# Performance work log

Hardware: AMD Instinct MI355X
Metric: run time of the kernel (lower is better)

The kernel has to match this reference:

```python
import jax, jax.numpy as jnp
import numpy as np

N = 50000
E = 800000
IN_C = 128
HID = 128
OUT_C = 2


def _linear_params(key, fan_in, fan_out):
    k1, k2 = jax.random.split(key)
    bound = 1.0 / np.sqrt(fan_in)
    W = jax.random.uniform(k1, (fan_in, fan_out), jnp.float32, -bound, bound)
    b = jax.random.uniform(k2, (fan_out,), jnp.float32, -bound, bound)
    return W, b


def setup_inputs() -> dict:
    key = jax.random.key(0)
    ks = jax.random.split(key, 9)
    x = jax.random.normal(ks[0], (N, IN_C), jnp.float32)
    edge_index = jax.random.randint(ks[1], (2, E), 0, N, jnp.int64)
    W1a, b1a = _linear_params(ks[2], IN_C, HID)
    W1b, b1b = _linear_params(ks[3], HID, HID)
    W2a, b2a = _linear_params(ks[4], HID, HID)
    W2b, b2b = _linear_params(ks[5], HID, HID)
    Wfc, bfc = _linear_params(ks[6], HID, OUT_C)
    return {
        "x": x, "edge_index": edge_index,
        "W1a": W1a, "b1a": b1a, "W1b": W1b, "b1b": b1b,
        "W2a": W2a, "b2a": b2a, "W2b": W2b, "b2b": b2b,
        "Wfc": Wfc, "bfc": bfc,
    }


def _gin_conv(x, src, dst, Wa, ba, Wb, bb):
    # GINConv with eps=0: h = MLP(x + sum_{j in N(i)} x_j)
    agg = jax.ops.segment_sum(x[src], dst, num_segments=N)  # [N, d]
    h = x + agg
    h = jax.nn.relu(h @ Wa + ba)
    return h @ Wb + bb


def reference(x, edge_index, W1a, b1a, W1b, b1b, W2a, b2a, W2b, b2b, Wfc, bfc):
    src, dst = edge_index[0], edge_index[1]  # messages flow src -> dst
    h = _gin_conv(x, src, dst, W1a, b1a, W1b, b1b)
    h = jax.nn.relu(h)
    # dropout is identity in eval mode
    h = _gin_conv(h, src, dst, W2a, b2a, W2b, b2b)
    return h @ Wfc + bfc  # [N, 2]
```

## Files before the change

### kernel.cpp

```cpp
#include <hip/hip_runtime.h>

#define N_NODES 50000
#define N_EDGES 800000
#define NBUK    392
#define B_A     1024
#define EPB     782
#define CAPB    2560

typedef unsigned short u16;
typedef unsigned int   u32;
typedef __bf16 bf16x8 __attribute__((ext_vector_type(8)));
typedef float  f32x4  __attribute__((ext_vector_type(4)));

__device__ __forceinline__ float bf_lo(u32 v){ return __uint_as_float(v << 16); }
__device__ __forceinline__ float bf_hi(u32 v){ return __uint_as_float(v & 0xffff0000u); }
__device__ __forceinline__ u32 bf_pack(float a, float b){
    u32 ua = __float_as_uint(a), ub = __float_as_uint(b);
    ua += 0x7fffu + ((ua >> 16) & 1u);
    ub += 0x7fffu + ((ub >> 16) & 1u);
    return (ua >> 16) | (ub & 0xffff0000u);
}
__device__ __forceinline__ u16 f2bf(float a){
    u32 ua = __float_as_uint(a);
    ua += 0x7fffu + ((ua >> 16) & 1u);
    return (u16)(ua >> 16);
}
__device__ __forceinline__ void addu4(uint4 v, float* a){
    a[0] += bf_lo(v.x); a[1] += bf_hi(v.x);
    a[2] += bf_lo(v.y); a[3] += bf_hi(v.y);
    a[4] += bf_lo(v.z); a[5] += bf_hi(v.z);
    a[6] += bf_lo(v.w); a[7] += bf_hi(v.w);
}

__device__ __forceinline__ int blockScan256(int v, int* ws, int t) {
    int lane = t & 63, w = t >> 6;
    #pragma unroll
    for (int off = 1; off < 64; off <<= 1) {
        int u = __shfl_up(v, off);
        if (lane >= off) v += u;
    }
    if (lane == 63) ws[w] = v;
    __syncthreads();
    int add = 0;
    for (int k = 0; k < w; k++) add += ws[k];
    return v + add;
}

__launch_bounds__(256)
__global__ void binA_kernel(const int* __restrict__ esrc, const int* __restrict__ edst,
                            u32* __restrict__ binned, int* __restrict__ startTab,
                            int* __restrict__ cntTab,
                            const float* __restrict__ xsrc, u32* __restrict__ xb,
                            const float* __restrict__ W1a, const float* __restrict__ W1b,
                            const float* __restrict__ W2a, const float* __restrict__ W2b,
                            const float* __restrict__ Wfc, const float* __restrict__ b2b,
                            const float* __restrict__ bfc,
                            u16* __restrict__ wt1a, u16* __restrict__ wt1b,
                            u16* __restrict__ wt2a,
                            float* __restrict__ Wc, float* __restrict__ bc) {
    int t = threadIdx.x, blk = blockIdx.x;
    if (blk >= B_A) {
        int b = blk - B_A;
        if (b < 192) {
            int g  = b * 256 + t;
            int mi = g >> 14;
            int p  = g & 16383;
            int k  = p >> 7, m = p & 127;
            const float* src = (mi == 0) ? W1a : (mi == 1) ? W1b : W2a;
            u16* dst         = (mi == 0) ? wt1a : (mi == 1) ? wt1b : wt2a;
            dst[m * 128 + k] = f2bf(src[k * 128 + m]);
        } else {
            int j = t >> 1, o = t & 1;
            float s = 0.f;
            for (int k = 0; k < 128; k++)
                s += W2b[j * 128 + k] * Wfc[k * 2 + o];
            Wc[j * 2 + o] = s;
            if (t < 2) {
                float s2 = 0.f;
                for (int k = 0; k < 128; k++)
                    s2 += b2b[k] * Wfc[k * 2 + t];
                bc[t] = s2 + bfc[t];
            }
        }
        return;
    }
    __shared__ int hist[NBUK];
    __shared__ int cur[NBUK];
    __shared__ u32 ebuf[EPB];
    __shared__ int ws[4];
    int base = blk * EPB;
    for (int i = t; i < NBUK; i += 256) hist[i] = 0;
    __syncthreads();
    for (int i = t; i < EPB; i += 256) {
        int gi = base + i;
        if (gi < N_EDGES) atomicAdd(&hist[edst[gi] >> 7], 1);
    }
    __syncthreads();
    int c0 = 0, c1 = 0;
    if (t < 196) { c0 = hist[2 * t]; c1 = hist[2 * t + 1]; }
    int s2 = c0 + c1;
    int incl = blockScan256(s2, ws, t);
    int excl = incl - s2;
    if (t < 196) {
        startTab[(2 * t) * B_A + blk]     = excl;
        cntTab[(2 * t) * B_A + blk]       = c0;
        cur[2 * t] = excl;
        startTab[(2 * t + 1) * B_A + blk] = excl + c0;
        cntTab[(2 * t + 1) * B_A + blk]   = c1;
        cur[2 * t + 1] = excl + c0;
    }
    __syncthreads();
    for (int i = t; i < EPB; i += 256) {
        int gi = base + i;
        if (gi < N_EDGES) {
            int d = edst[gi], s = esrc[gi];
            int p = atomicAdd(&cur[d >> 7], 1);
            ebuf[p] = (u32)s | ((u32)(d & 127) << 16);
        }
    }
    __syncthreads();
    for (int i = t; i < EPB; i += 256)
        binned[base + i] = ebuf[i];
    const int total = N_NODES * 64;
    for (int i = blk * 256 + t; i < total; i += B_A * 256) {
        float2 f = ((const float2*)xsrc)[i];
        xb[i] = bf_pack(f.x, f.y);
    }
}

__launch_bounds__(256)
__global__ void binB_kernel(const u32* __restrict__ binned, const int* __restrict__ startTab,
                            const int* __restrict__ cntTab,
                            int2* __restrict__ span, int* __restrict__ csr) {
    __shared__ u32 ebuf[CAPB];
    __shared__ int cbuf[CAPB];
    __shared__ int hist[128];
    __shared__ int cursor[128];
    __shared__ int ws[4];
    __shared__ int totsh;
    int b = blockIdx.x, t = threadIdx.x;
    int c4[4], rs4[4], s = 0;
    #pragma unroll
    for (int q = 0; q < 4; q++) {
        int run = t * 4 + q;
        c4[q]  = cntTab[b * B_A + run];
        rs4[q] = run * EPB + startTab[b * B_A + run];
        s += c4[q];
    }
    int incl = blockScan256(s, ws, t);
    int rb = incl - s;
    if (t == 255) totsh = incl;
    if (t < 128) hist[t] = 0;
    __syncthreads();
    #pragma unroll
    for (int q = 0; q < 4; q++) {
        int c = c4[q], rs = rs4[q];
        for (int k = 0; k < c; k++) {
            int p = rb + k;
            if (p < CAPB) ebuf[p] = binned[rs + k];
        }
        rb += c;
    }
    __syncthreads();
    int tot = totsh;
    if (tot > CAPB) tot = CAPB;
    for (int i = t; i < tot; i += 256)
        atomicAdd(&hist[ebuf[i] >> 16], 1);
    __syncthreads();
    int hv = (t < 128) ? hist[t] : 0;
    int hincl = blockScan256(hv, ws, t);
    int hexcl = hincl - hv;
    int gb = b * CAPB;
    if (t < 128) {
        cursor[t] = hexcl;
        int node = (b << 7) + t;
        if (node < N_NODES) span[node] = make_int2(gb + hexcl, gb + hexcl + hv);
    }
    __syncthreads();
    for (int i = t; i < tot; i += 256) {
        u32 e = ebuf[i];
        int p = atomicAdd(&cursor[e >> 16], 1);
        cbuf[p] = (int)(e & 0xFFFFu);
    }
    __syncthreads();
    for (int i = t; i < tot; i += 256)
        csr[gb + i] = cbuf[i];
}

template<int MODE>
__launch_bounds__(256, 4)
__global__ void fconv_kernel(const u32* __restrict__ xb,
                             const u16* __restrict__ WA, const float* __restrict__ bA,
                             const u16* __restrict__ WB, const float* __restrict__ bB,
                             const float* __restrict__ Wc, const float* __restrict__ bc,
                             const int2* __restrict__ span, const int* __restrict__ csr,
                             u16* __restrict__ C, float2* __restrict__ out, int n) {
    __shared__ u16 As[64][136];
    int t = threadIdx.x;
    int row0 = blockIdx.x * 64;
    int w = t >> 6, lane = t & 63;
    int g4 = lane >> 4, l16 = lane & 15;
    const uint4* xp = (const uint4*)xb;
    #pragma unroll
    for (int p = 0; p < 4; p++) {
        int rl = w * 16 + p * 4 + g4;
        int node = row0 + rl;
        float a[8] = {0.f,0.f,0.f,0.f,0.f,0.f,0.f,0.f};
        if (node < n) {
            addu4(xp[(size_t)node * 16 + l16], a);
            int2 sp = span[node];
            int j = sp.x, jend = sp.y;
            for (; j + 8 <= jend; j += 8) {
                int s0 = csr[j],     s1 = csr[j + 1], s2 = csr[j + 2], s3 = csr[j + 3];
                int s4 = csr[j + 4], s5 = csr[j + 5], s6 = csr[j + 6], s7 = csr[j + 7];
                uint4 v0 = xp[(size_t)s0 * 16 + l16], v1 = xp[(size_t)s1 * 16 + l16];
                uint4 v2 = xp[(size_t)s2 * 16 + l16], v3 = xp[(size_t)s3 * 16 + l16];
                uint4 v4 = xp[(size_t)s4 * 16 + l16], v5 = xp[(size_t)s5 * 16 + l16];
                uint4 v6 = xp[(size_t)s6 * 16 + l16], v7 = xp[(size_t)s7 * 16 + l16];
                addu4(v0, a); addu4(v1, a); addu4(v2, a); addu4(v3, a);
                addu4(v4, a); addu4(v5, a); addu4(v6, a); addu4(v7, a);
            }
            for (; j + 4 <= jend; j += 4) {
                int s0 = csr[j], s1 = csr[j + 1], s2 = csr[j + 2], s3 = csr[j + 3];
                uint4 v0 = xp[(size_t)s0 * 16 + l16], v1 = xp[(size_t)s1 * 16 + l16];
                uint4 v2 = xp[(size_t)s2 * 16 + l16], v3 = xp[(size_t)s3 * 16 + l16];
                addu4(v0, a); addu4(v1, a); addu4(v2, a); addu4(v3, a);
            }
            for (; j < jend; j++)
                addu4(xp[(size_t)csr[j] * 16 + l16], a);
        }
        uint4 pk = make_uint4(bf_pack(a[0], a[1]), bf_pack(a[2], a[3]),
                              bf_pack(a[4], a[5]), bf_pack(a[6], a[7]));
        *(uint4*)&As[rl][l16 * 8] = pk;
    }

    int lm = l16, lq = g4;
    f32x4 acc[8];
    #pragma unroll
    for (int c = 0; c < 8; c++) acc[c] = (f32x4){0.f, 0.f, 0.f, 0.f};
    #pragma unroll
    for (int kk = 0; kk < 4; kk++) {
        bf16x8 af = *(const bf16x8*)&As[w * 16 + lm][kk * 32 + lq * 8];
        #pragma unroll
        for (int c = 0; c < 8; c++) {
            bf16x8 bf = *(const bf16x8*)(WA + (size_t)(c * 16 + lm) * 128 + kk * 32 + lq * 8);
            acc[c] = __builtin_amdgcn_mfma_f32_16x16x32_bf16(af, bf, acc[c], 0, 0, 0);
        }
    }
    if (MODE == 0) {
        #pragma unroll
        for (int c = 0; c < 8; c++) {
            int col = c * 16 + lm;
            float bcol = bA[col];
            #pragma unroll
            for (int r = 0; r < 4; r++) {
                float v = acc[c][r] + bcol;
                v = v > 0.f ? v : 0.f;
                As[w * 16 + lq * 4 + r][col] = f2bf(v);
            }
        }
        f32x4 acc2[8];
        #pragma unroll
        for (int c = 0; c < 8; c++) acc2[c] = (f32x4){0.f, 0.f, 0.f, 0.f};
        #pragma unroll
        for (int kk = 0; kk < 4; kk++) {
            bf16x8 af = *(const bf16x8*)&As[w * 16 + lm][kk * 32 + lq * 8];
            #pragma unroll
            for (int c = 0; c < 8; c++) {
                bf16x8 bf = *(const bf16x8*)(WB + (size_t)(c * 16 + lm) * 128 + kk * 32 + lq * 8);
                acc2[c] = __builtin_amdgcn_mfma_f32_16x16x32_bf16(af, bf, acc2[c], 0, 0, 0);
            }
        }
        #pragma unroll
        for (int c = 0; c < 8; c++) {
            int col = c * 16 + lm;
            float bcol = bB[col];
            #pragma unroll
            for (int r = 0; r < 4; r++) {
                int row = row0 + w * 16 + lq * 4 + r;
                if (row < n) {
                    float v = acc2[c][r] + bcol;
                    v = v > 0.f ? v : 0.f;
                    C[(size_t)row * 128 + col] = f2bf(v);
                }
            }
        }
    } else {
        float p0[4] = {0,0,0,0}, p1[4] = {0,0,0,0};
        #pragma unroll
        for (int c = 0; c < 8; c++) {
            int col = c * 16 + lm;
            float bcol = bA[col];
            float2 wc = ((const float2*)Wc)[col];
            #pragma unroll
            for (int r = 0; r < 4; r++) {
                float v = acc[c][r] + bcol;
                v = v > 0.f ? v : 0.f;
                p0[r] += v * wc.x;
                p1[r] += v * wc.y;
            }
        }
        #pragma unroll
        for (int off = 1; off < 16; off <<= 1) {
            #pragma unroll
            for (int r = 0; r < 4; r++) {
                p0[r] += __shfl_xor(p0[r], off);
                p1[r] += __shfl_xor(p1[r], off);
            }
        }
        if (lm == 0) {
            float b0 = bc[0], b1 = bc[1];
            #pragma unroll
            for (int r = 0; r < 4; r++) {
                int row = row0 + w * 16 + lq * 4 + r;
                if (row < n) out[row] = make_float2(p0[r] + b0, p1[r] + b1);
            }
        }
    }
}

extern "C" void kernel_launch(void* const* d_in, const int* in_sizes, int n_in,
                              void* d_out, int out_size, void* d_ws, size_t ws_size,
                              hipStream_t stream) {
    const float* x   = (const float*)d_in[0];
    const int*   ei  = (const int*)d_in[1];
    const float* W1a = (const float*)d_in[2];
    const float* b1a = (const float*)d_in[3];
    const float* W1b = (const float*)d_in[4];
    const float* b1b = (const float*)d_in[5];
    const float* W2a = (const float*)d_in[6];
    const float* b2a = (const float*)d_in[7];
    const float* W2b = (const float*)d_in[8];
    const float* b2b = (const float*)d_in[9];
    const float* Wfc = (const float*)d_in[10];
    const float* bfc = (const float*)d_in[11];

    const int* esrc = ei;
    const int* edst = ei + N_EDGES;

    char* w = (char*)d_ws;
    size_t off = 0;
    auto alloc = [&](size_t bytes) -> char* {
        char* p = w + off;
        off = (off + bytes + 255) & ~(size_t)255;
        return p;
    };
    int2*  span       = (int2*)alloc((size_t)N_NODES * 8);
    int*   startTab   = (int*)alloc((size_t)NBUK * B_A * 4);
    int*   cntTab     = (int*)alloc((size_t)NBUK * B_A * 4);
    int*   csr        = (int*)alloc((size_t)NBUK * CAPB * 4);
    u16*   wt1a       = (u16*)alloc(128 * 128 * 2);
    u16*   wt1b       = (u16*)alloc(128 * 128 * 2);
    u16*   wt2a       = (u16*)alloc(128 * 128 * 2);
    float* Wc         = (float*)alloc(256 * 4);
    float* bc         = (float*)alloc(2 * 4);
    u16*   bufA       = (u16*)alloc((size_t)N_NODES * 128 * 2);
    u16*   bufB       = (u16*)alloc((size_t)N_NODES * 128 * 2);
    u32*   binned     = (u32*)bufA;

    binA_kernel<<<B_A + 193, 256, 0, stream>>>(esrc, edst, binned, startTab, cntTab,
                                               x, (u32*)bufB,
                                               W1a, W1b, W2a, W2b, Wfc, b2b, bfc,
                                               wt1a, wt1b, wt2a, Wc, bc);
    binB_kernel<<<NBUK, 256, 0, stream>>>(binned, startTab, cntTab, span, csr);

    const int TILES = (N_NODES + 63) / 64;
    fconv_kernel<0><<<TILES, 256, 0, stream>>>((const u32*)bufB, wt1a, b1a, wt1b, b1b,
                                               nullptr, nullptr, span, csr,
                                               bufA, nullptr, N_NODES);
    fconv_kernel<1><<<TILES, 256, 0, stream>>>((const u32*)bufA, wt2a, b2a, nullptr, nullptr,
                                               Wc, bc, span, csr,
                                               nullptr, (float2*)d_out, N_NODES);
}
```

Measured before the change: 223.7 us.

## Fuse CSR bucket build with first GIN conv in one kernel

The bucket-sort kernel that builds the per-bucket CSR is merged with the layer-1 aggregation and two-layer MLP. Each 512-thread block sorts its 128 nodes' edges in shared memory, then gathers neighbours straight from the shared CSR instead of rereading it from global memory, removing one launch and one round trip. The global CSR and span arrays are still written for layer 2. The binned edge list gets its own workspace buffer, because bufA is now written in the same kernel that reads it. The trade-off is fewer, larger blocks (392 of 512 threads) with heavier shared-memory use, which may change how well gather latency is hidden.

```diff
diff --git a/kernel.cpp b/kernel.cpp
--- a/kernel.cpp
+++ b/kernel.cpp
@@ -33,6 +33,20 @@
 }
 
 __device__ __forceinline__ int blockScan256(int v, int* ws, int t) {
+    int lane = t & 63, w = t >> 6;
+    #pragma unroll
+    for (int off = 1; off < 64; off <<= 1) {
+        int u = __shfl_up(v, off);
+        if (lane >= off) v += u;
+    }
+    if (lane == 63) ws[w] = v;
+    __syncthreads();
+    int add = 0;
+    for (int k = 0; k < w; k++) add += ws[k];
+    return v + add;
+}
+
+__device__ __forceinline__ int blockScan512(int v, int* ws, int t) {
     int lane = t & 63, w = t >> 6;
     #pragma unroll
     for (int off = 1; off < 64; off <<= 1) {
@@ -128,33 +142,40 @@
     }
 }
 
-__launch_bounds__(256)
-__global__ void binB_kernel(const u32* __restrict__ binned, const int* __restrict__ startTab,
-                            const int* __restrict__ cntTab,
-                            int2* __restrict__ span, int* __restrict__ csr) {
-    __shared__ u32 ebuf[CAPB];
-    __shared__ int cbuf[CAPB];
-    __shared__ int hist[128];
-    __shared__ int cursor[128];
-    __shared__ int ws[4];
-    __shared__ int totsh;
+__launch_bounds__(512, 4)
+__global__ void bconv1_kernel(const u32* __restrict__ binned,
+                              const int* __restrict__ startTab, const int* __restrict__ cntTab,
+                              const u32* __restrict__ xb,
+                              const u16* __restrict__ WA, const float* __restrict__ bA,
+                              const u16* __restrict__ WB, const float* __restrict__ bB,
+                              int2* __restrict__ span, int* __restrict__ csr,
+                              u16* __restrict__ h1, int n) {
+    __shared__ __align__(16) char shbuf[34816 + 10240 + 512 + 512 + 32 + 16];
+    u16 (*As)[136] = (u16(*)[136])shbuf;
+    u32* ebuf      = (u32*)shbuf;
+    int* cbuf      = (int*)(shbuf + 34816);
+    int* hist      = (int*)(shbuf + 34816 + 10240);
+    int* cursor    = (int*)(shbuf + 34816 + 10240 + 512);
+    int* ws        = (int*)(shbuf + 34816 + 10240 + 1024);
+    int* totsh     = ws + 8;
     int b = blockIdx.x, t = threadIdx.x;
-    int c4[4], rs4[4], s = 0;
-    #pragma unroll
-    for (int q = 0; q < 4; q++) {
-        int run = t * 4 + q;
-        c4[q]  = cntTab[b * B_A + run];
-        rs4[q] = run * EPB + startTab[b * B_A + run];
-        s += c4[q];
-    }
-    int incl = blockScan256(s, ws, t);
+
+    int c2[2], rs2[2], s = 0;
+    #pragma unroll
+    for (int q = 0; q < 2; q++) {
+        int run = t * 2 + q;
+        c2[q]  = cntTab[b * B_A + run];
+        rs2[q] = run * EPB + startTab[b * B_A + run];
+        s += c2[q];
+    }
+    int incl = blockScan512(s, ws, t);
     int rb = incl - s;
-    if (t == 255) totsh = incl;
+    if (t == 511) *totsh = incl;
     if (t < 128) hist[t] = 0;
     __syncthreads();
     #pragma unroll
-    for (int q = 0; q < 4; q++) {
-        int c = c4[q], rs = rs4[q];
+    for (int q = 0; q < 2; q++) {
+        int c = c2[q], rs = rs2[q];
         for (int k = 0; k < c; k++) {
             int p = rb + k;
             if (p < CAPB) ebuf[p] = binned[rs + k];
@@ -162,39 +183,125 @@
         rb += c;
     }
     __syncthreads();
-    int tot = totsh;
+    int tot = *totsh;
     if (tot > CAPB) tot = CAPB;
-    for (int i = t; i < tot; i += 256)
+    for (int i = t; i < tot; i += 512)
         atomicAdd(&hist[ebuf[i] >> 16], 1);
     __syncthreads();
     int hv = (t < 128) ? hist[t] : 0;
-    int hincl = blockScan256(hv, ws, t);
+    int hincl = blockScan512(hv, ws, t);
     int hexcl = hincl - hv;
     int gb = b * CAPB;
     if (t < 128) {
+        hist[t]   = hexcl;
         cursor[t] = hexcl;
         int node = (b << 7) + t;
-        if (node < N_NODES) span[node] = make_int2(gb + hexcl, gb + hexcl + hv);
-    }
-    __syncthreads();
-    for (int i = t; i < tot; i += 256) {
+        if (node < n) span[node] = make_int2(gb + hexcl, gb + hexcl + hv);
+    }
+    __syncthreads();
+    for (int i = t; i < tot; i += 512) {
         u32 e = ebuf[i];
         int p = atomicAdd(&cursor[e >> 16], 1);
         cbuf[p] = (int)(e & 0xFFFFu);
     }
     __syncthreads();
-    for (int i = t; i < tot; i += 256)
+    for (int i = t; i < tot; i += 512)
         csr[gb + i] = cbuf[i];
-}
-
-template<int MODE>
+    __syncthreads();
+
+    int row0 = b * 128;
+    int w = t >> 6, lane = t & 63;
+    int g4 = lane >> 4, l16 = lane & 15;
+    const uint4* xp = (const uint4*)xb;
+    #pragma unroll
+    for (int p = 0; p < 4; p++) {
+        int rl = w * 16 + p * 4 + g4;
+        int node = row0 + rl;
+        float a[8] = {0.f,0.f,0.f,0.f,0.f,0.f,0.f,0.f};
+        if (node < n) {
+            addu4(xp[(size_t)node * 16 + l16], a);
+            int j = hist[rl], jend = cursor[rl];
+            for (; j + 8 <= jend; j += 8) {
+                int s0 = cbuf[j],     s1 = cbuf[j + 1], s2b = cbuf[j + 2], s3 = cbuf[j + 3];
+                int s4 = cbuf[j + 4], s5 = cbuf[j + 5], s6 = cbuf[j + 6], s7 = cbuf[j + 7];
+                uint4 v0 = xp[(size_t)s0 * 16 + l16], v1 = xp[(size_t)s1 * 16 + l16];
+                uint4 v2 = xp[(size_t)s2b * 16 + l16], v3 = xp[(size_t)s3 * 16 + l16];
+                uint4 v4 = xp[(size_t)s4 * 16 + l16], v5 = xp[(size_t)s5 * 16 + l16];
+                uint4 v6 = xp[(size_t)s6 * 16 + l16], v7 = xp[(size_t)s7 * 16 + l16];
+                addu4(v0, a); addu4(v1, a); addu4(v2, a); addu4(v3, a);
+                addu4(v4, a); addu4(v5, a); addu4(v6, a); addu4(v7, a);
+            }
+            for (; j + 4 <= jend; j += 4) {
+                int s0 = cbuf[j], s1 = cbuf[j + 1], s2b = cbuf[j + 2], s3 = cbuf[j + 3];
+                uint4 v0 = xp[(size_t)s0 * 16 + l16], v1 = xp[(size_t)s1 * 16 + l16];
+                uint4 v2 = xp[(size_t)s2b * 16 + l16], v3 = xp[(size_t)s3 * 16 + l16];
+                addu4(v0, a); addu4(v1, a); addu4(v2, a); addu4(v3, a);
+            }
+            for (; j < jend; j++)
+                addu4(xp[(size_t)cbuf[j] * 16 + l16], a);
+        }
+        uint4 pk = make_uint4(bf_pack(a[0], a[1]), bf_pack(a[2], a[3]),
+                              bf_pack(a[4], a[5]), bf_pack(a[6], a[7]));
+        *(uint4*)&As[rl][l16 * 8] = pk;
+    }
+    int lm = l16, lq = g4;
+    f32x4 acc[8];
+    #pragma unroll
+    for (int c = 0; c < 8; c++) acc[c] = (f32x4){0.f, 0.f, 0.f, 0.f};
+    #pragma unroll
+    for (int kk = 0; kk < 4; kk++) {
+        bf16x8 af = *(const bf16x8*)&As[w * 16 + lm][kk * 32 + lq * 8];
+        #pragma unroll
+        for (int c = 0; c < 8; c++) {
+            bf16x8 bf = *(const bf16x8*)(WA + (size_t)(c * 16 + lm) * 128 + kk * 32 + lq * 8);
+            acc[c] = __builtin_amdgcn_mfma_f32_16x16x32_bf16(af, bf, acc[c], 0, 0, 0);
+        }
+    }
+    #pragma unroll
+    for (int c = 0; c < 8; c++) {
+        int col = c * 16 + lm;
+        float bcol = bA[col];
+        #pragma unroll
+        for (int r = 0; r < 4; r++) {
+            float v = acc[c][r] + bcol;
+            v = v > 0.f ? v : 0.f;
+            As[w * 16 + lq * 4 + r][col] = f2bf(v);
+        }
+    }
+    f32x4 acc2[8];
+    #pragma unroll
+    for (int c = 0; c < 8; c++) acc2[c] = (f32x4){0.f, 0.f, 0.f, 0.f};
+    #pragma unroll
+    for (int kk = 0; kk < 4; kk++) {
+        bf16x8 af = *(const bf16x8*)&As[w * 16 + lm][kk * 32 + lq * 8];
+        #pragma unroll
+        for (int c = 0; c < 8; c++) {
+            bf16x8 bf = *(const bf16x8*)(WB + (size_t)(c * 16 + lm) * 128 + kk * 32 + lq * 8);
+            acc2[c] = __builtin_amdgcn_mfma_f32_16x16x32_bf16(af, bf, acc2[c], 0, 0, 0);
+        }
+    }
+    #pragma unroll
+    for (int c = 0; c < 8; c++) {
+        int col = c * 16 + lm;
+        float bcol = bB[col];
+        #pragma unroll
+        for (int r = 0; r < 4; r++) {
+            int row = row0 + w * 16 + lq * 4 + r;
+            if (row < n) {
+                float v = acc2[c][r] + bcol;
+                v = v > 0.f ? v : 0.f;
+                h1[(size_t)row * 128 + col] = f2bf(v);
+            }
+        }
+    }
+}
+
 __launch_bounds__(256, 4)
-__global__ void fconv_kernel(const u32* __restrict__ xb,
-                             const u16* __restrict__ WA, const float* __restrict__ bA,
-                             const u16* __restrict__ WB, const float* __restrict__ bB,
-                             const float* __restrict__ Wc, const float* __restrict__ bc,
-                             const int2* __restrict__ span, const int* __restrict__ csr,
-                             u16* __restrict__ C, float2* __restrict__ out, int n) {
+__global__ void fconv2_kernel(const u32* __restrict__ xb,
+                              const u16* __restrict__ WA, const float* __restrict__ bA,
+                              const float* __restrict__ Wc, const float* __restrict__ bc,
+                              const int2* __restrict__ span, const int* __restrict__ csr,
+                              float2* __restrict__ out, int n) {
     __shared__ u16 As[64][136];
     int t = threadIdx.x;
     int row0 = blockIdx.x * 64;
@@ -233,7 +340,6 @@
                               bf_pack(a[4], a[5]), bf_pack(a[6], a[7]));
         *(uint4*)&As[rl][l16 * 8] = pk;
     }
-
     int lm = l16, lq = g4;
     f32x4 acc[8];
     #pragma unroll
@@ -247,74 +353,34 @@
             acc[c] = __builtin_amdgcn_mfma_f32_16x16x32_bf16(af, bf, acc[c], 0, 0, 0);
         }
     }
-    if (MODE == 0) {
-        #pragma unroll
-        for (int c = 0; c < 8; c++) {
-            int col = c * 16 + lm;
-            float bcol = bA[col];
-            #pragma unroll
-            for (int r = 0; r < 4; r++) {
-                float v = acc[c][r] + bcol;
-                v = v > 0.f ? v : 0.f;
-                As[w * 16 + lq * 4 + r][col] = f2bf(v);
-            }
-        }
-        f32x4 acc2[8];
-        #pragma unroll
-        for (int c = 0; c < 8; c++) acc2[c] = (f32x4){0.f, 0.f, 0.f, 0.f};
-        #pragma unroll
-        for (int kk = 0; kk < 4; kk++) {
-            bf16x8 af = *(const bf16x8*)&As[w * 16 + lm][kk * 32 + lq * 8];
-            #pragma unroll
-            for (int c = 0; c < 8; c++) {
-                bf16x8 bf = *(const bf16x8*)(WB + (size_t)(c * 16 + lm) * 128 + kk * 32 + lq * 8);
-                acc2[c] = __builtin_amdgcn_mfma_f32_16x16x32_bf16(af, bf, acc2[c], 0, 0, 0);
-            }
-        }
-        #pragma unroll
-        for (int c = 0; c < 8; c++) {
-            int col = c * 16 + lm;
-            float bcol = bB[col];
-            #pragma unroll
-            for (int r = 0; r < 4; r++) {
-                int row = row0 + w * 16 + lq * 4 + r;
-                if (row < n) {
-                    float v = acc2[c][r] + bcol;
-                    v = v > 0.f ? v : 0.f;
-                    C[(size_t)row * 128 + col] = f2bf(v);
-                }
-            }
-        }
-    } else {
-        float p0[4] = {0,0,0,0}, p1[4] = {0,0,0,0};
-        #pragma unroll
-        for (int c = 0; c < 8; c++) {
-            int col = c * 16 + lm;
-            float bcol = bA[col];
-            float2 wc = ((const float2*)Wc)[col];
-            #pragma unroll
-            for (int r = 0; r < 4; r++) {
-                float v = acc[c][r] + bcol;
-                v = v > 0.f ? v : 0.f;
-                p0[r] += v * wc.x;
-                p1[r] += v * wc.y;
-            }
-        }
-        #pragma unroll
-        for (int off = 1; off < 16; off <<= 1) {
-            #pragma unroll
-            for (int r = 0; r < 4; r++) {
-                p0[r] += __shfl_xor(p0[r], off);
-                p1[r] += __shfl_xor(p1[r], off);
-            }
-        }
-        if (lm == 0) {
-            float b0 = bc[0], b1 = bc[1];
-            #pragma unroll
-            for (int r = 0; r < 4; r++) {
-                int row = row0 + w * 16 + lq * 4 + r;
-                if (row < n) out[row] = make_float2(p0[r] + b0, p1[r] + b1);
-            }
+    float p0[4] = {0,0,0,0}, p1[4] = {0,0,0,0};
+    #pragma unroll
+    for (int c = 0; c < 8; c++) {
+        int col = c * 16 + lm;
+        float bcol = bA[col];
+        float2 wc = ((const float2*)Wc)[col];
+        #pragma unroll
+        for (int r = 0; r < 4; r++) {
+            float v = acc[c][r] + bcol;
+            v = v > 0.f ? v : 0.f;
+            p0[r] += v * wc.x;
+            p1[r] += v * wc.y;
+        }
+    }
+    #pragma unroll
+    for (int off = 1; off < 16; off <<= 1) {
+        #pragma unroll
+        for (int r = 0; r < 4; r++) {
+            p0[r] += __shfl_xor(p0[r], off);
+            p1[r] += __shfl_xor(p1[r], off);
+        }
+    }
+    if (lm == 0) {
+        float b0 = bc[0], b1 = bc[1];
+        #pragma unroll
+        for (int r = 0; r < 4; r++) {
+            int row = row0 + w * 16 + lq * 4 + r;
+            if (row < n) out[row] = make_float2(p0[r] + b0, p1[r] + b1);
         }
     }
 }
@@ -349,6 +415,7 @@
     int*   startTab   = (int*)alloc((size_t)NBUK * B_A * 4);
     int*   cntTab     = (int*)alloc((size_t)NBUK * B_A * 4);
     int*   csr        = (int*)alloc((size_t)NBUK * CAPB * 4);
+    u32*   binned     = (u32*)alloc((size_t)B_A * EPB * 4);
     u16*   wt1a       = (u16*)alloc(128 * 128 * 2);
     u16*   wt1b       = (u16*)alloc(128 * 128 * 2);
     u16*   wt2a       = (u16*)alloc(128 * 128 * 2);
@@ -356,19 +423,15 @@
     float* bc         = (float*)alloc(2 * 4);
     u16*   bufA       = (u16*)alloc((size_t)N_NODES * 128 * 2);
     u16*   bufB       = (u16*)alloc((size_t)N_NODES * 128 * 2);
-    u32*   binned     = (u32*)bufA;
 
     binA_kernel<<<B_A + 193, 256, 0, stream>>>(esrc, edst, binned, startTab, cntTab,
                                                x, (u32*)bufB,
                                                W1a, W1b, W2a, W2b, Wfc, b2b, bfc,
                                                wt1a, wt1b, wt2a, Wc, bc);
-    binB_kernel<<<NBUK, 256, 0, stream>>>(binned, startTab, cntTab, span, csr);
-
-    const int TILES = (N_NODES + 63) / 64;
-    fconv_kernel<0><<<TILES, 256, 0, stream>>>((const u32*)bufB, wt1a, b1a, wt1b, b1b,
-                                               nullptr, nullptr, span, csr,
-                                               bufA, nullptr, N_NODES);
-    fconv_kernel<1><<<TILES, 256, 0, stream>>>((const u32*)bufA, wt2a, b2a, nullptr, nullptr,
-                                               Wc, bc, span, csr,
-                                               nullptr, (float2*)d_out, N_NODES);
-}
+    bconv1_kernel<<<NBUK, 512, 0, stream>>>(binned, startTab, cntTab,
+                                            (const u32*)bufB, wt1a, b1a, wt1b, b1b,
+                                            span, csr, bufA, N_NODES);
+    fconv2_kernel<<<(N_NODES + 63) / 64, 256, 0, stream>>>((const u32*)bufA, wt2a, b2a,
+                                                           Wc, bc, span, csr,
+                                                           (float2*)d_out, N_NODES);
+}
```

New measurement: 210.0 us, median of 2. -6.1%, faster.

## Split aggregation from GEMMs and store features in 32-channel slabs

Applied to the files above, without the earlier changes.

Feature matrices are now stored as four column slabs of 32 channels each. The gather-sum is split out into its own kernel, and each block works on one slab for two 64-node tiles, ordered so that blocks sharing a slab run close together. The aim is to shrink the working set of each gather so the randomly accessed neighbour rows stay in cache, and to raise occupancy for the memory-bound phase. The cost is two extra kernel launches and a write and re-read of the aggregated tensor through global memory.

```diff
diff --git a/kernel.cpp b/kernel.cpp
--- a/kernel.cpp
+++ b/kernel.cpp
@@ -6,6 +6,9 @@
 #define B_A     1024
 #define EPB     782
 #define CAPB    2560
+#define SLAB32  (N_NODES * 16)
+#define SLAB16  (N_NODES * 32)
+#define TILES   782
 
 typedef unsigned short u16;
 typedef unsigned int   u32;
@@ -124,7 +127,8 @@
     const int total = N_NODES * 64;
     for (int i = blk * 256 + t; i < total; i += B_A * 256) {
         float2 f = ((const float2*)xsrc)[i];
-        xb[i] = bf_pack(f.x, f.y);
+        int node = i >> 6, c2 = i & 63;
+        xb[(c2 >> 4) * SLAB32 + node * 16 + (c2 & 15)] = bf_pack(f.x, f.y);
     }
 }
 
@@ -187,54 +191,58 @@
         csr[gb + i] = cbuf[i];
 }
 
-template<int MODE>
+__launch_bounds__(256, 8)
+__global__ void agg_kernel(const u32* __restrict__ xb,
+                           const int2* __restrict__ span, const int* __restrict__ csr,
+                           u32* __restrict__ outb, int n) {
+    int i = blockIdx.x;
+    int k = i & 7;
+    int slab = k & 3;
+    int tile = (i >> 3) * 2 + (k >> 2);
+    int t = threadIdx.x;
+    int w = t >> 6, lane = t & 63;
+    int sub = lane >> 2, ch = lane & 3;
+    int node = tile * 64 + w * 16 + sub;
+    if (node >= n) return;
+    const uint4* sp = (const uint4*)(xb + (size_t)slab * SLAB32);
+    int2 spn = span[node];
+    int j = spn.x, jend = spn.y;
+    float a[8] = {0.f,0.f,0.f,0.f,0.f,0.f,0.f,0.f};
+    addu4(sp[(size_t)node * 4 + ch], a);
+    for (; j + 4 <= jend; j += 4) {
+        int s0 = csr[j], s1 = csr[j + 1], s2 = csr[j + 2], s3 = csr[j + 3];
+        uint4 v0 = sp[(size_t)s0 * 4 + ch], v1 = sp[(size_t)s1 * 4 + ch];
+        uint4 v2 = sp[(size_t)s2 * 4 + ch], v3 = sp[(size_t)s3 * 4 + ch];
+        addu4(v0, a); addu4(v1, a); addu4(v2, a); addu4(v3, a);
+    }
+    for (; j < jend; j++)
+        addu4(sp[(size_t)csr[j] * 4 + ch], a);
+    uint4 pk = make_uint4(bf_pack(a[0], a[1]), bf_pack(a[2], a[3]),
+                          bf_pack(a[4], a[5]), bf_pack(a[6], a[7]));
+    ((uint4*)(outb + (size_t)slab * SLAB32))[(size_t)node * 4 + ch] = pk;
+}
+
 __launch_bounds__(256, 4)
-__global__ void fconv_kernel(const u32* __restrict__ xb,
+__global__ void gemm1_kernel(const u32* __restrict__ A,
                              const u16* __restrict__ WA, const float* __restrict__ bA,
                              const u16* __restrict__ WB, const float* __restrict__ bB,
-                             const float* __restrict__ Wc, const float* __restrict__ bc,
-                             const int2* __restrict__ span, const int* __restrict__ csr,
-                             u16* __restrict__ C, float2* __restrict__ out, int n) {
+                             u16* __restrict__ h1, int n) {
     __shared__ u16 As[64][136];
     int t = threadIdx.x;
     int row0 = blockIdx.x * 64;
+    {
+        int rl = t >> 2, q = t & 3;
+        int node = row0 + rl;
+        #pragma unroll
+        for (int slab = 0; slab < 4; slab++) {
+            uint4 v = make_uint4(0, 0, 0, 0);
+            if (node < n) v = ((const uint4*)(A + (size_t)slab * SLAB32))[(size_t)node * 4 + q];
+            *(uint4*)&As[rl][slab * 32 + q * 8] = v;
+        }
+    }
+    __syncthreads();
     int w = t >> 6, lane = t & 63;
-    int g4 = lane >> 4, l16 = lane & 15;
-    const uint4* xp = (const uint4*)xb;
-    #pragma unroll
-    for (int p = 0; p < 4; p++) {
-        int rl = w * 16 + p * 4 + g4;
-        int node = row0 + rl;
-        float a[8] = {0.f,0.f,0.f,0.f,0.f,0.f,0.f,0.f};
-        if (node < n) {
-            addu4(xp[(size_t)node * 16 + l16], a);
-            int2 sp = span[node];
-            int j = sp.x, jend = sp.y;
-            for (; j + 8 <= jend; j += 8) {
-                int s0 = csr[j],     s1 = csr[j + 1], s2 = csr[j + 2], s3 = csr[j + 3];
-                int s4 = csr[j + 4], s5 = csr[j + 5], s6 = csr[j + 6], s7 = csr[j + 7];
-                uint4 v0 = xp[(size_t)s0 * 16 + l16], v1 = xp[(size_t)s1 * 16 + l16];
-                uint4 v2 = xp[(size_t)s2 * 16 + l16], v3 = xp[(size_t)s3 * 16 + l16];
-                uint4 v4 = xp[(size_t)s4 * 16 + l16], v5 = xp[(size_t)s5 * 16 + l16];
-                uint4 v6 = xp[(size_t)s6 * 16 + l16], v7 = xp[(size_t)s7 * 16 + l16];
-                addu4(v0, a); addu4(v1, a); addu4(v2, a); addu4(v3, a);
-                addu4(v4, a); addu4(v5, a); addu4(v6, a); addu4(v7, a);
-            }
-            for (; j + 4 <= jend; j += 4) {
-                int s0 = csr[j], s1 = csr[j + 1], s2 = csr[j + 2], s3 = csr[j + 3];
-                uint4 v0 = xp[(size_t)s0 * 16 + l16], v1 = xp[(size_t)s1 * 16 + l16];
-                uint4 v2 = xp[(size_t)s2 * 16 + l16], v3 = xp[(size_t)s3 * 16 + l16];
-                addu4(v0, a); addu4(v1, a); addu4(v2, a); addu4(v3, a);
-            }
-            for (; j < jend; j++)
-                addu4(xp[(size_t)csr[j] * 16 + l16], a);
-        }
-        uint4 pk = make_uint4(bf_pack(a[0], a[1]), bf_pack(a[2], a[3]),
-                              bf_pack(a[4], a[5]), bf_pack(a[6], a[7]));
-        *(uint4*)&As[rl][l16 * 8] = pk;
-    }
-
-    int lm = l16, lq = g4;
+    int lm = lane & 15, lq = lane >> 4;
     f32x4 acc[8];
     #pragma unroll
     for (int c = 0; c < 8; c++) acc[c] = (f32x4){0.f, 0.f, 0.f, 0.f};
@@ -247,74 +255,107 @@
             acc[c] = __builtin_amdgcn_mfma_f32_16x16x32_bf16(af, bf, acc[c], 0, 0, 0);
         }
     }
-    if (MODE == 0) {
+    #pragma unroll
+    for (int c = 0; c < 8; c++) {
+        int col = c * 16 + lm;
+        float bcol = bA[col];
+        #pragma unroll
+        for (int r = 0; r < 4; r++) {
+            float v = acc[c][r] + bcol;
+            v = v > 0.f ? v : 0.f;
+            As[w * 16 + lq * 4 + r][col] = f2bf(v);
+        }
+    }
+    f32x4 acc2[8];
+    #pragma unroll
+    for (int c = 0; c < 8; c++) acc2[c] = (f32x4){0.f, 0.f, 0.f, 0.f};
+    #pragma unroll
+    for (int kk = 0; kk < 4; kk++) {
+        bf16x8 af = *(const bf16x8*)&As[w * 16 + lm][kk * 32 + lq * 8];
         #pragma unroll
         for (int c = 0; c < 8; c++) {
-            int col = c * 16 + lm;
-            float bcol = bA[col];
-            #pragma unroll
-            for (int r = 0; r < 4; r++) {
-                float v = acc[c][r] + bcol;
+            bf16x8 bf = *(const bf16x8*)(WB + (size_t)(c * 16 + lm) * 128 + kk * 32 + lq * 8);
+            acc2[c] = __builtin_amdgcn_mfma_f32_16x16x32_bf16(af, bf, acc2[c], 0, 0, 0);
+        }
+    }
+    #pragma unroll
+    for (int c = 0; c < 8; c++) {
+        int col = c * 16 + lm;
+        float bcol = bB[col];
+        int slab = col >> 5, cw = col & 31;
+        #pragma unroll
+        for (int r = 0; r < 4; r++) {
+            int row = row0 + w * 16 + lq * 4 + r;
+            if (row < n) {
+                float v = acc2[c][r] + bcol;
                 v = v > 0.f ? v : 0.f;
-                As[w * 16 + lq * 4 + r][col] = f2bf(v);
+                h1[(size_t)slab * SLAB16 + (size_t)row * 32 + cw] = f2bf(v);
             }
         }
-        f32x4 acc2[8];
-        #pragma unroll
-        for (int c = 0; c < 8; c++) acc2[c] = (f32x4){0.f, 0.f, 0.f, 0.f};
-        #pragma unroll
-        for (int kk = 0; kk < 4; kk++) {
-            bf16x8 af = *(const bf16x8*)&As[w * 16 + lm][kk * 32 + lq * 8];
-            #pragma unroll
-            for (int c = 0; c < 8; c++) {
-                bf16x8 bf = *(const bf16x8*)(WB + (size_t)(c * 16 + lm) * 128 + kk * 32 + lq * 8);
-                acc2[c] = __builtin_amdgcn_mfma_f32_16x16x32_bf16(af, bf, acc2[c], 0, 0, 0);
-            }
-        }
+    }
+}
+
+__launch_bounds__(256, 4)
+__global__ void gemm2fc_kernel(const u32* __restrict__ A,
+                               const u16* __restrict__ WA, const float* __restrict__ bA,
+                               const float* __restrict__ Wc, const float* __restrict__ bc,
+                               float2* __restrict__ out, int n) {
+    __shared__ u16 As[64][136];
+    int t = threadIdx.x;
+    int row0 = blockIdx.x * 64;
+    {
+        int rl = t >> 2, q = t & 3;
+        int node = row0 + rl;
+        #pragma unroll
+        for (int slab = 0; slab < 4; slab++) {
+            uint4 v = make_uint4(0, 0, 0, 0);
+            if (node < n) v = ((const uint4*)(A + (size_t)slab * SLAB32))[(size_t)node * 4 + q];
+            *(uint4*)&As[rl][slab * 32 + q * 8] = v;
+        }
+    }
+    __syncthreads();
+    int w = t >> 6, lane = t & 63;
+    int lm = lane & 15, lq = lane >> 4;
+    f32x4 acc[8];
+    #pragma unroll
+    for (int c = 0; c < 8; c++) acc[c] = (f32x4){0.f, 0.f, 0.f, 0.f};
+    #pragma unroll
+    for (int kk = 0; kk < 4; kk++) {
+        bf16x8 af = *(const bf16x8*)&As[w * 16 + lm][kk * 32 + lq * 8];
         #pragma unroll
         for (int c = 0; c < 8; c++) {
-            int col = c * 16 + lm;
-            float bcol = bB[col];
-            #pragma unroll
-            for (int r = 0; r < 4; r++) {
-                int row = row0 + w * 16 + lq * 4 + r;
-                if (row < n) {
-                    float v = acc2[c][r] + bcol;
-                    v = v > 0.f ? v : 0.f;
-                    C[(size_t)row * 128 + col] = f2bf(v);
-                }
-            }
-        }
-    } else {
-        float p0[4] = {0,0,0,0}, p1[4] = {0,0,0,0};
-        #pragma unroll
-        for (int c = 0; c < 8; c++) {
-            int col = c * 16 + lm;
-            float bcol = bA[col];
-            float2 wc = ((const float2*)Wc)[col];
-            #pragma unroll
-            for (int r = 0; r < 4; r++) {
-                float v = acc[c][r] + bcol;
-                v = v > 0.f ? v : 0.f;
-                p0[r] += v * wc.x;
-                p1[r] += v * wc.y;
-            }
-        }
-        #pragma unroll
-        for (int off = 1; off < 16; off <<= 1) {
-            #pragma unroll
-            for (int r = 0; r < 4; r++) {
-                p0[r] += __shfl_xor(p0[r], off);
-                p1[r] += __shfl_xor(p1[r], off);
-            }
-        }
-        if (lm == 0) {
-            float b0 = bc[0], b1 = bc[1];
-            #pragma unroll
-            for (int r = 0; r < 4; r++) {
-                int row = row0 + w * 16 + lq * 4 + r;
-                if (row < n) out[row] = make_float2(p0[r] + b0, p1[r] + b1);
-            }
+            bf16x8 bf = *(const bf16x8*)(WA + (size_t)(c * 16 + lm) * 128 + kk * 32 + lq * 8);
+            acc[c] = __builtin_amdgcn_mfma_f32_16x16x32_bf16(af, bf, acc[c], 0, 0, 0);
+        }
+    }
+    float p0[4] = {0,0,0,0}, p1[4] = {0,0,0,0};
+    #pragma unroll
+    for (int c = 0; c < 8; c++) {
+        int col = c * 16 + lm;
+        float bcol = bA[col];
+        float2 wc = ((const float2*)Wc)[col];
+        #pragma unroll
+        for (int r = 0; r < 4; r++) {
+            float v = acc[c][r] + bcol;
+            v = v > 0.f ? v : 0.f;
+            p0[r] += v * wc.x;
+            p1[r] += v * wc.y;
+        }
+    }
+    #pragma unroll
+    for (int off = 1; off < 16; off <<= 1) {
+        #pragma unroll
+        for (int r = 0; r < 4; r++) {
+            p0[r] += __shfl_xor(p0[r], off);
+            p1[r] += __shfl_xor(p1[r], off);
+        }
+    }
+    if (lm == 0) {
+        float b0 = bc[0], b1 = bc[1];
+        #pragma unroll
+        for (int r = 0; r < 4; r++) {
+            int row = row0 + w * 16 + lq * 4 + r;
+            if (row < n) out[row] = make_float2(p0[r] + b0, p1[r] + b1);
         }
     }
 }
@@ -349,26 +390,24 @@
     int*   startTab   = (int*)alloc((size_t)NBUK * B_A * 4);
     int*   cntTab     = (int*)alloc((size_t)NBUK * B_A * 4);
     int*   csr        = (int*)alloc((size_t)NBUK * CAPB * 4);
+    u32*   binned     = (u32*)alloc((size_t)B_A * EPB * 4);
     u16*   wt1a       = (u16*)alloc(128 * 128 * 2);
     u16*   wt1b       = (u16*)alloc(128 * 128 * 2);
     u16*   wt2a       = (u16*)alloc(128 * 128 * 2);
     float* Wc         = (float*)alloc(256 * 4);
     float* bc         = (float*)alloc(2 * 4);
-    u16*   bufA       = (u16*)alloc((size_t)N_NODES * 128 * 2);
-    u16*   bufB       = (u16*)alloc((size_t)N_NODES * 128 * 2);
-    u32*   binned     = (u32*)bufA;
+    u32*   xb         = (u32*)alloc((size_t)N_NODES * 64 * 4);
+    u32*   aggA       = (u32*)alloc((size_t)N_NODES * 64 * 4);
+    u16*   h1         = (u16*)alloc((size_t)N_NODES * 128 * 2);
 
     binA_kernel<<<B_A + 193, 256, 0, stream>>>(esrc, edst, binned, startTab, cntTab,
-                                               x, (u32*)bufB,
+                                               x, xb,
                                                W1a, W1b, W2a, W2b, Wfc, b2b, bfc,
                                                wt1a, wt1b, wt2a, Wc, bc);
     binB_kernel<<<NBUK, 256, 0, stream>>>(binned, startTab, cntTab, span, csr);
-
-    const int TILES = (N_NODES + 63) / 64;
-    fconv_kernel<0><<<TILES, 256, 0, stream>>>((const u32*)bufB, wt1a, b1a, wt1b, b1b,
-                                               nullptr, nullptr, span, csr,
-                                               bufA, nullptr, N_NODES);
-    fconv_kernel<1><<<TILES, 256, 0, stream>>>((const u32*)bufA, wt2a, b2a, nullptr, nullptr,
-                                               Wc, bc, span, csr,
-                                               nullptr, (float2*)d_out, N_NODES);
-}
+    agg_kernel<<<3128, 256, 0, stream>>>(xb, span, csr, aggA, N_NODES);
+    gemm1_kernel<<<TILES, 256, 0, stream>>>(aggA, wt1a, b1a, wt1b, b1b, h1, N_NODES);
+    agg_kernel<<<3128, 256, 0, stream>>>((const u32*)h1, span, csr, aggA, N_NODES);
+    gemm2fc_kernel<<<TILES, 256, 0, stream>>>(aggA, wt2a, b2a, Wc, bc,
+                                              (float2*)d_out, N_NODES);
+}
```

New measurement: 228.6 us. +2.2%, slower.
